# Optimization experiments

Measured on AMD Instinct MI355X. Metric: run time of the kernel, lower is better.

The kernel has to match this reference:

```python
import jax, jax.numpy as jnp
import numpy as np

B, C, H, W = 8, 128, 256, 256
WS = 8          # window_size (square)
HEADS = 4


def setup_inputs() -> dict:
    key = jax.random.key(0)
    k1, k2, k3, k4 = jax.random.split(key, 4)
    x = jax.random.normal(k1, (B, C, H, W), dtype=jnp.float32)
    # 1x1 convs are per-pixel matmuls; store weights as [out, in]
    w_qkv = jax.random.normal(k2, (3 * C, C), dtype=jnp.float32) * 0.05   # qkv conv, bias=False
    w_proj = jax.random.normal(k3, (C, C), dtype=jnp.float32) * 0.05      # proj conv weight
    b_proj = jax.random.normal(k4, (C,), dtype=jnp.float32) * 0.01        # proj conv bias
    return {"x": x, "w_qkv": w_qkv, "w_proj": w_proj, "b_proj": b_proj}


def reference(x, w_qkv, w_proj, b_proj):
    b, c, h, w = x.shape
    ws, heads = WS, HEADS
    d = c // heads
    scale = d ** -0.5
    hn, wn = h // ws, w // ws
    n = ws * ws  # tokens per window

    # unfold with kernel=stride=ws -> row-major window partition
    # [B,C,H,W] -> [B*hn*wn, C, n]
    xw = x.reshape(b, c, hn, ws, wn, ws)
    xw = xw.transpose(0, 2, 4, 1, 3, 5).reshape(b * hn * wn, c, n)

    # 1x1 conv QKV projection (no bias)
    qkv = jnp.einsum('oc,bcn->bon', w_qkv, xw)  # [Bw, 3C, n]
    q, k, v = jnp.split(qkv, 3, axis=1)
    q = q.reshape(-1, heads, d, n)
    k = k.reshape(-1, heads, d, n)
    v = v.reshape(-1, heads, d, n)

    # attn = (q^T k) * scale, softmax over keys
    attn = jax.nn.softmax(jnp.einsum('bhdn,bhdm->bhnm', q, k) * scale, axis=-1)
    out = jnp.einsum('bhnm,bhdm->bhdn', attn, v).reshape(-1, c, n)  # [Bw, C, n]

    # 1x1 proj conv with bias
    out = jnp.einsum('oc,bcn->bon', w_proj, out) + b_proj[None, :, None]

    # fold windows back: [Bw, C, n] -> [B, C, H, W]
    out = out.reshape(b, hn, wn, c, ws, ws)
    out = out.transpose(0, 3, 1, 4, 2, 5).reshape(b, c, h, w)
    return out
```

## Files before the change

kernel.cpp:

```cpp
#include <hip/hip_runtime.h>


#define HH    256
#define WWID  256
#define SCALE 0.17677669529663687f
#define LOG2E 1.44269504088896340736f

typedef float  f32x4  __attribute__((ext_vector_type(4)));
typedef __bf16 bf16x8 __attribute__((ext_vector_type(8)));
typedef __bf16 bf16x4 __attribute__((ext_vector_type(4)));
typedef __bf16 bf16x2 __attribute__((ext_vector_type(2)));
typedef short  s16x4  __attribute__((ext_vector_type(4)));

#define OT_BASE 16384

__device__ __forceinline__ s16x4 pack4(f32x4 v) {
  bf16x4 b = {(__bf16)v[0], (__bf16)v[1], (__bf16)v[2], (__bf16)v[3]};
  return __builtin_bit_cast(s16x4, b);
}

#if __has_builtin(__builtin_amdgcn_mfma_f32_16x16x16bf16_1k)
__device__ __forceinline__ f32x4 mfma16(s16x4 a, s16x4 b, f32x4 c) {
  return __builtin_amdgcn_mfma_f32_16x16x16bf16_1k(a, b, c, 0, 0, 0);
}
#else
__device__ __forceinline__ f32x4 mfma16(s16x4 a, s16x4 b, f32x4 c) {
  asm("v_mfma_f32_16x16x16_bf16 %0, %1, %2, %0" : "+v"(c) : "v"(a), "v"(b));
  return c;
}
#endif

__global__ void prep_weights(const float* __restrict__ wqkv,
                             const float* __restrict__ wproj,
                             __bf16* __restrict__ wbf) {
  int i = blockIdx.x * 256 + threadIdx.x;
  float v = (i < 49152) ? wqkv[i] : wproj[i - 49152];
  if (i < 16384) v *= SCALE * LOG2E;
  wbf[i] = (__bf16)v;
}

__global__ __launch_bounds__(256, 2)
void winattn_main(const float* __restrict__ x,
                  const __bf16* __restrict__ wqkv,
                  const __bf16* __restrict__ wproj,
                  const float* __restrict__ bproj,
                  float* __restrict__ out) {
  __shared__ __align__(16) char smem[32768];

  const int tid  = threadIdx.x;
  const int lane = tid & 63;
  const int wv   = tid >> 6;
  const int l15  = lane & 15;
  const int l4   = lane >> 4;

  const int bid = blockIdx.x;
  const int win = ((bid & 7) << 10) | (bid >> 3);
  const int b   = win >> 10;
  const int wy  = (win >> 5) & 31;
  const int wx  = win & 31;
  const int gy0 = wy * 8, gx0 = wx * 8;

  #pragma unroll
  for (int it = 0; it < 4; ++it) {
    int idx   = tid + it * 256;
    int cpair = idx >> 4;
    int r     = idx & 15;
    int ty    = r >> 1, tx4 = r & 1;
    const float* px = x + (((size_t)(b * 128 + 2 * cpair) * HH + gy0 + ty) * WWID + gx0 + tx4 * 4);
    float4 v0 = *(const float4*)px;
    float4 v1 = *(const float4*)(px + (size_t)HH * WWID);
    float a0[4] = {v0.x, v0.y, v0.z, v0.w};
    float a1[4] = {v1.x, v1.y, v1.z, v1.w};
    #pragma unroll
    for (int i = 0; i < 4; ++i) {
      int tok = ty * 8 + tx4 * 4 + i;
      bf16x2 w2 = {(__bf16)a0[i], (__bf16)a1[i]};
      int byte = (tok * 256 + cpair * 4) ^ ((tok & 15) << 4);
      *(bf16x2*)(smem + byte) = w2;
    }
  }
  __syncthreads();

  #define XT_AFRAG(mt, kt) \
    (*(const bf16x8*)(smem + ((((mt) * 16 + l15) * 256 + ((kt) * 32 + l4 * 8) * 2) ^ \
                              ((((mt) * 16 + l15) & 15) << 4))))
  #define OT_AFRAG(mt, kt) \
    (*(const bf16x8*)(smem + OT_BASE + ((((mt) * 16 + l15) * 256 + ((kt) * 32 + l4 * 8) * 2) ^ \
                              ((((mt) * 16 + l15) & 15) << 4))))

  s16x4 qb[2][4], kb[2][4];
  {
    f32x4 accQ[2][4] = {}, accK[2][4] = {};
    #pragma unroll
    for (int kt = 0; kt < 4; ++kt) {
      bf16x8 xf[4];
      #pragma unroll
      for (int mt = 0; mt < 4; ++mt) xf[mt] = XT_AFRAG(mt, kt);
      #pragma unroll
      for (int nt2 = 0; nt2 < 2; ++nt2) {
        bf16x8 wq = *(const bf16x8*)(wqkv + (size_t)(wv * 32 + nt2 * 16 + l15) * 128 + kt * 32 + l4 * 8);
        bf16x8 wk = *(const bf16x8*)(wqkv + (size_t)(128 + wv * 32 + nt2 * 16 + l15) * 128 + kt * 32 + l4 * 8);
        #pragma unroll
        for (int mt = 0; mt < 4; ++mt) {
          accQ[nt2][mt] = __builtin_amdgcn_mfma_f32_16x16x32_bf16(wq, xf[mt], accQ[nt2][mt], 0, 0, 0);
          accK[nt2][mt] = __builtin_amdgcn_mfma_f32_16x16x32_bf16(wk, xf[mt], accK[nt2][mt], 0, 0, 0);
        }
      }
    }
    #pragma unroll
    for (int nt2 = 0; nt2 < 2; ++nt2)
      #pragma unroll
      for (int mt = 0; mt < 4; ++mt) {
        qb[nt2][mt] = pack4(accQ[nt2][mt]);
        kb[nt2][mt] = pack4(accK[nt2][mt]);
      }
  }

  s16x4 vb[2][4];
  {
    f32x4 accV[2][4] = {};
    #pragma unroll
    for (int kt = 0; kt < 4; ++kt) {
      bf16x8 xf[4];
      #pragma unroll
      for (int mt = 0; mt < 4; ++mt) xf[mt] = XT_AFRAG(mt, kt);
      #pragma unroll
      for (int nt2 = 0; nt2 < 2; ++nt2) {
        bf16x8 wf = *(const bf16x8*)(wqkv + (size_t)(256 + wv * 32 + nt2 * 16 + l15) * 128 + kt * 32 + l4 * 8);
        #pragma unroll
        for (int mt = 0; mt < 4; ++mt)
          accV[nt2][mt] = __builtin_amdgcn_mfma_f32_16x16x32_bf16(xf[mt], wf, accV[nt2][mt], 0, 0, 0);
      }
    }
    #pragma unroll
    for (int nt2 = 0; nt2 < 2; ++nt2)
      #pragma unroll
      for (int mt = 0; mt < 4; ++mt) vb[nt2][mt] = pack4(accV[nt2][mt]);
  }

  f32x4 oacc[4][2] = {};
  #pragma unroll
  for (int t = 0; t < 4; ++t) {
    f32x4 st[4];
    #pragma unroll
    for (int m = 0; m < 4; ++m) {
      f32x4 z = {0.f, 0.f, 0.f, 0.f};
      st[m] = mfma16(kb[0][m], qb[0][t], z);
      st[m] = mfma16(kb[1][m], qb[1][t], st[m]);
    }
    float mx = st[0][0];
    #pragma unroll
    for (int m = 0; m < 4; ++m)
      #pragma unroll
      for (int r = 0; r < 4; ++r) mx = fmaxf(mx, st[m][r]);
    mx = fmaxf(mx, __shfl_xor(mx, 16));
    mx = fmaxf(mx, __shfl_xor(mx, 32));
    float p[4][4];
    float sm = 0.f;
    #pragma unroll
    for (int m = 0; m < 4; ++m)
      #pragma unroll
      for (int r = 0; r < 4; ++r) {
        p[m][r] = __builtin_amdgcn_exp2f(st[m][r] - mx);
        sm += p[m][r];
      }
    sm += __shfl_xor(sm, 16);
    sm += __shfl_xor(sm, 32);
    float inv = __builtin_amdgcn_rcpf(sm);
    s16x4 ap[4];
    #pragma unroll
    for (int m = 0; m < 4; ++m) {
      f32x4 pn = {p[m][0] * inv, p[m][1] * inv, p[m][2] * inv, p[m][3] * inv};
      ap[m] = pack4(pn);
    }
    #pragma unroll
    for (int m = 0; m < 4; ++m)
      #pragma unroll
      for (int n = 0; n < 2; ++n)
        oacc[t][n] = mfma16(ap[m], vb[n][m], oacc[t][n]);
  }

  #pragma unroll
  for (int t = 0; t < 4; ++t)
    #pragma unroll
    for (int n = 0; n < 2; ++n)
      #pragma unroll
      for (int r = 0; r < 4; ++r) {
        int tok  = t * 16 + l4 * 4 + r;
        int c    = wv * 32 + n * 16 + l15;
        int byte = OT_BASE + ((tok * 256 + c * 2) ^ ((tok & 15) << 4));
        *(__bf16*)(smem + byte) = (__bf16)oacc[t][n][r];
      }
  __syncthreads();

  f32x4 pacc[2][4] = {};
  #pragma unroll
  for (int kt = 0; kt < 4; ++kt) {
    bf16x8 of[4];
    #pragma unroll
    for (int mt = 0; mt < 4; ++mt) of[mt] = OT_AFRAG(mt, kt);
    #pragma unroll
    for (int i = 0; i < 2; ++i) {
      bf16x8 wp = *(const bf16x8*)(wproj + (size_t)((wv * 2 + i) * 16 + l15) * 128 + kt * 32 + l4 * 8);
      #pragma unroll
      for (int mt = 0; mt < 4; ++mt)
        pacc[i][mt] = __builtin_amdgcn_mfma_f32_16x16x32_bf16(of[mt], wp, pacc[i][mt], 0, 0, 0);
    }
  }

  #pragma unroll
  for (int i = 0; i < 2; ++i) {
    int o = (wv * 2 + i) * 16 + l15;
    float bias = bproj[o];
    float* obase = out + (size_t)(b * 128 + o) * ((size_t)HH * WWID) + gy0 * WWID + gx0;
    #pragma unroll
    for (int mt = 0; mt < 4; ++mt) {
      int tok0 = mt * 16 + l4 * 4;
      int ty = tok0 >> 3, tx0 = tok0 & 7;
      float4 f = {pacc[i][mt][0] + bias, pacc[i][mt][1] + bias,
                  pacc[i][mt][2] + bias, pacc[i][mt][3] + bias};
      *(float4*)(obase + ty * WWID + tx0) = f;
    }
  }
}

extern "C" void kernel_launch(void* const* d_in, const int* in_sizes, int n_in,
                              void* d_out, int out_size, void* d_ws, size_t ws_size,
                              hipStream_t stream) {
  const float* x     = (const float*)d_in[0];
  const float* wqkv  = (const float*)d_in[1];
  const float* wproj = (const float*)d_in[2];
  const float* bproj = (const float*)d_in[3];
  float* out = (float*)d_out;

  __bf16* wbf = (__bf16*)d_ws;
  prep_weights<<<256, 256, 0, stream>>>(wqkv, wproj, wbf);
  winattn_main<<<8192, 256, 0, stream>>>(x, wbf, wbf + 49152, bproj, out);
}
```

Measured before the change: 261.0 us.

## Process four windows per block with double-buffered prefetch of next window

Each block now handles four consecutive windows instead of one, cutting the grid from 8192 to 2048 blocks. The next window's input is loaded into registers while the projection GEMM of the current window runs, then written into an alternate LDS buffer. The attention output is stored to LDS per row tile instead of being kept in accumulators, which lowers register pressure. The cost is more LDS per block (48KB), which may reduce occupancy, plus extra barriers and a longer serial chain inside each block.

```diff
diff --git a/kernel.cpp b/kernel.cpp
--- a/kernel.cpp
+++ b/kernel.cpp
@@ -12,7 +12,7 @@
 typedef __bf16 bf16x2 __attribute__((ext_vector_type(2)));
 typedef short  s16x4  __attribute__((ext_vector_type(4)));
 
-#define OT_BASE 16384
+#define OT_BASE 32768
 
 __device__ __forceinline__ s16x4 pack4(f32x4 v) {
   bf16x4 b = {(__bf16)v[0], (__bf16)v[1], (__bf16)v[2], (__bf16)v[3]};
@@ -45,7 +45,7 @@
                   const __bf16* __restrict__ wproj,
                   const float* __restrict__ bproj,
                   float* __restrict__ out) {
-  __shared__ __align__(16) char smem[32768];
+  __shared__ __align__(16) char smem[49152];
 
   const int tid  = threadIdx.x;
   const int lane = tid & 63;
@@ -54,172 +54,205 @@
   const int l4   = lane >> 4;
 
   const int bid = blockIdx.x;
-  const int win = ((bid & 7) << 10) | (bid >> 3);
-  const int b   = win >> 10;
-  const int wy  = (win >> 5) & 31;
-  const int wx  = win & 31;
-  const int gy0 = wy * 8, gx0 = wx * 8;
-
+  const int b   = bid & 7;
+  const int grp = bid >> 3;
+
+  int tcpair[4], tty[4], ttx4[4];
   #pragma unroll
   for (int it = 0; it < 4; ++it) {
-    int idx   = tid + it * 256;
-    int cpair = idx >> 4;
-    int r     = idx & 15;
-    int ty    = r >> 1, tx4 = r & 1;
-    const float* px = x + (((size_t)(b * 128 + 2 * cpair) * HH + gy0 + ty) * WWID + gx0 + tx4 * 4);
-    float4 v0 = *(const float4*)px;
-    float4 v1 = *(const float4*)(px + (size_t)HH * WWID);
-    float a0[4] = {v0.x, v0.y, v0.z, v0.w};
-    float a1[4] = {v1.x, v1.y, v1.z, v1.w};
-    #pragma unroll
-    for (int i = 0; i < 4; ++i) {
-      int tok = ty * 8 + tx4 * 4 + i;
-      bf16x2 w2 = {(__bf16)a0[i], (__bf16)a1[i]};
-      int byte = (tok * 256 + cpair * 4) ^ ((tok & 15) << 4);
-      *(bf16x2*)(smem + byte) = w2;
-    }
+    int idx = tid + it * 256;
+    tcpair[it] = idx >> 4;
+    int r = idx & 15;
+    tty[it] = r >> 1;
+    ttx4[it] = r & 1;
   }
-  __syncthreads();
-
-  #define XT_AFRAG(mt, kt) \
-    (*(const bf16x8*)(smem + ((((mt) * 16 + l15) * 256 + ((kt) * 32 + l4 * 8) * 2) ^ \
+
+  #define ISSUE_LOADS(widx, pv0, pv1)                                              \
+    {                                                                              \
+      int gy0_ = ((widx) >> 5) * 8, gx0_ = ((widx) & 31) * 8;                      \
+      _Pragma("unroll")                                                            \
+      for (int it = 0; it < 4; ++it) {                                             \
+        const float* px = x + (((size_t)(b * 128 + 2 * tcpair[it]) * HH + gy0_ +   \
+                                tty[it]) * WWID + gx0_ + ttx4[it] * 4);            \
+        pv0[it] = *(const float4*)px;                                              \
+        pv1[it] = *(const float4*)(px + (size_t)HH * WWID);                        \
+      }                                                                            \
+    }
+
+  #define STORE_TILE(pv0, pv1, base)                                               \
+    {                                                                              \
+      _Pragma("unroll")                                                            \
+      for (int it = 0; it < 4; ++it) {                                             \
+        float a0_[4] = {pv0[it].x, pv0[it].y, pv0[it].z, pv0[it].w};               \
+        float a1_[4] = {pv1[it].x, pv1[it].y, pv1[it].z, pv1[it].w};               \
+        _Pragma("unroll")                                                          \
+        for (int i = 0; i < 4; ++i) {                                              \
+          int tok = tty[it] * 8 + ttx4[it] * 4 + i;                                \
+          bf16x2 w2 = {(__bf16)a0_[i], (__bf16)a1_[i]};                            \
+          int byte = (base) + ((tok * 256 + tcpair[it] * 4) ^ ((tok & 15) << 4));  \
+          *(bf16x2*)(smem + byte) = w2;                                            \
+        }                                                                          \
+      }                                                                            \
+    }
+
+  #define XT_AFRAG(base, mt, kt) \
+    (*(const bf16x8*)(smem + (base) + ((((mt) * 16 + l15) * 256 + ((kt) * 32 + l4 * 8) * 2) ^ \
                               ((((mt) * 16 + l15) & 15) << 4))))
   #define OT_AFRAG(mt, kt) \
     (*(const bf16x8*)(smem + OT_BASE + ((((mt) * 16 + l15) * 256 + ((kt) * 32 + l4 * 8) * 2) ^ \
                               ((((mt) * 16 + l15) & 15) << 4))))
 
-  s16x4 qb[2][4], kb[2][4];
   {
-    f32x4 accQ[2][4] = {}, accK[2][4] = {};
+    float4 pv0[4], pv1[4];
+    ISSUE_LOADS(grp * 4, pv0, pv1);
+    STORE_TILE(pv0, pv1, 0);
+  }
+  __syncthreads();
+
+  #pragma unroll
+  for (int w = 0; w < 4; ++w) {
+    const int XB = (w & 1) ? 16384 : 0;
+    const int NB = XB ^ 16384;
+    const int widx = grp * 4 + w;
+    const int gy0 = (widx >> 5) * 8, gx0 = (widx & 31) * 8;
+
+    s16x4 qb[2][4], kb[2][4];
+    {
+      f32x4 accQ[2][4] = {}, accK[2][4] = {};
+      #pragma unroll
+      for (int kt = 0; kt < 4; ++kt) {
+        bf16x8 xf[4];
+        #pragma unroll
+        for (int mt = 0; mt < 4; ++mt) xf[mt] = XT_AFRAG(XB, mt, kt);
+        #pragma unroll
+        for (int nt2 = 0; nt2 < 2; ++nt2) {
+          bf16x8 wq = *(const bf16x8*)(wqkv + (size_t)(wv * 32 + nt2 * 16 + l15) * 128 + kt * 32 + l4 * 8);
+          bf16x8 wk = *(const bf16x8*)(wqkv + (size_t)(128 + wv * 32 + nt2 * 16 + l15) * 128 + kt * 32 + l4 * 8);
+          #pragma unroll
+          for (int mt = 0; mt < 4; ++mt) {
+            accQ[nt2][mt] = __builtin_amdgcn_mfma_f32_16x16x32_bf16(wq, xf[mt], accQ[nt2][mt], 0, 0, 0);
+            accK[nt2][mt] = __builtin_amdgcn_mfma_f32_16x16x32_bf16(wk, xf[mt], accK[nt2][mt], 0, 0, 0);
+          }
+        }
+      }
+      #pragma unroll
+      for (int nt2 = 0; nt2 < 2; ++nt2)
+        #pragma unroll
+        for (int mt = 0; mt < 4; ++mt) {
+          qb[nt2][mt] = pack4(accQ[nt2][mt]);
+          kb[nt2][mt] = pack4(accK[nt2][mt]);
+        }
+    }
+
+    s16x4 vb[2][4];
+    {
+      f32x4 accV[2][4] = {};
+      #pragma unroll
+      for (int kt = 0; kt < 4; ++kt) {
+        bf16x8 xf[4];
+        #pragma unroll
+        for (int mt = 0; mt < 4; ++mt) xf[mt] = XT_AFRAG(XB, mt, kt);
+        #pragma unroll
+        for (int nt2 = 0; nt2 < 2; ++nt2) {
+          bf16x8 wf = *(const bf16x8*)(wqkv + (size_t)(256 + wv * 32 + nt2 * 16 + l15) * 128 + kt * 32 + l4 * 8);
+          #pragma unroll
+          for (int mt = 0; mt < 4; ++mt)
+            accV[nt2][mt] = __builtin_amdgcn_mfma_f32_16x16x32_bf16(xf[mt], wf, accV[nt2][mt], 0, 0, 0);
+        }
+      }
+      #pragma unroll
+      for (int nt2 = 0; nt2 < 2; ++nt2)
+        #pragma unroll
+        for (int mt = 0; mt < 4; ++mt) vb[nt2][mt] = pack4(accV[nt2][mt]);
+    }
+
+    #pragma unroll
+    for (int t = 0; t < 4; ++t) {
+      f32x4 st[4];
+      #pragma unroll
+      for (int m = 0; m < 4; ++m) {
+        f32x4 z = {0.f, 0.f, 0.f, 0.f};
+        st[m] = mfma16(kb[0][m], qb[0][t], z);
+        st[m] = mfma16(kb[1][m], qb[1][t], st[m]);
+      }
+      float mx = st[0][0];
+      #pragma unroll
+      for (int m = 0; m < 4; ++m)
+        #pragma unroll
+        for (int r = 0; r < 4; ++r) mx = fmaxf(mx, st[m][r]);
+      mx = fmaxf(mx, __shfl_xor(mx, 16));
+      mx = fmaxf(mx, __shfl_xor(mx, 32));
+      float p[4][4];
+      float sm = 0.f;
+      #pragma unroll
+      for (int m = 0; m < 4; ++m)
+        #pragma unroll
+        for (int r = 0; r < 4; ++r) {
+          p[m][r] = __builtin_amdgcn_exp2f(st[m][r] - mx);
+          sm += p[m][r];
+        }
+      sm += __shfl_xor(sm, 16);
+      sm += __shfl_xor(sm, 32);
+      float inv = __builtin_amdgcn_rcpf(sm);
+      s16x4 ap[4];
+      #pragma unroll
+      for (int m = 0; m < 4; ++m) {
+        f32x4 pn = {p[m][0] * inv, p[m][1] * inv, p[m][2] * inv, p[m][3] * inv};
+        ap[m] = pack4(pn);
+      }
+      f32x4 o0 = {0.f, 0.f, 0.f, 0.f}, o1 = {0.f, 0.f, 0.f, 0.f};
+      #pragma unroll
+      for (int m = 0; m < 4; ++m) {
+        o0 = mfma16(ap[m], vb[0][m], o0);
+        o1 = mfma16(ap[m], vb[1][m], o1);
+      }
+      #pragma unroll
+      for (int r = 0; r < 4; ++r) {
+        int tok = t * 16 + l4 * 4 + r;
+        int c0  = wv * 32 + l15;
+        int sw  = (tok & 15) << 4;
+        *(__bf16*)(smem + OT_BASE + ((tok * 256 + c0 * 2) ^ sw))        = (__bf16)o0[r];
+        *(__bf16*)(smem + OT_BASE + ((tok * 256 + (c0 + 16) * 2) ^ sw)) = (__bf16)o1[r];
+      }
+    }
+    __syncthreads();
+
+    float4 pv0[4], pv1[4];
+    if (w < 3) ISSUE_LOADS(widx + 1, pv0, pv1);
+
+    f32x4 pacc[2][4] = {};
     #pragma unroll
     for (int kt = 0; kt < 4; ++kt) {
-      bf16x8 xf[4];
-      #pragma unroll
-      for (int mt = 0; mt < 4; ++mt) xf[mt] = XT_AFRAG(mt, kt);
-      #pragma unroll
-      for (int nt2 = 0; nt2 < 2; ++nt2) {
-        bf16x8 wq = *(const bf16x8*)(wqkv + (size_t)(wv * 32 + nt2 * 16 + l15) * 128 + kt * 32 + l4 * 8);
-        bf16x8 wk = *(const bf16x8*)(wqkv + (size_t)(128 + wv * 32 + nt2 * 16 + l15) * 128 + kt * 32 + l4 * 8);
-        #pragma unroll
-        for (int mt = 0; mt < 4; ++mt) {
-          accQ[nt2][mt] = __builtin_amdgcn_mfma_f32_16x16x32_bf16(wq, xf[mt], accQ[nt2][mt], 0, 0, 0);
-          accK[nt2][mt] = __builtin_amdgcn_mfma_f32_16x16x32_bf16(wk, xf[mt], accK[nt2][mt], 0, 0, 0);
-        }
-      }
-    }
-    #pragma unroll
-    for (int nt2 = 0; nt2 < 2; ++nt2)
-      #pragma unroll
-      for (int mt = 0; mt < 4; ++mt) {
-        qb[nt2][mt] = pack4(accQ[nt2][mt]);
-        kb[nt2][mt] = pack4(accK[nt2][mt]);
-      }
-  }
-
-  s16x4 vb[2][4];
-  {
-    f32x4 accV[2][4] = {};
-    #pragma unroll
-    for (int kt = 0; kt < 4; ++kt) {
-      bf16x8 xf[4];
-      #pragma unroll
-      for (int mt = 0; mt < 4; ++mt) xf[mt] = XT_AFRAG(mt, kt);
-      #pragma unroll
-      for (int nt2 = 0; nt2 < 2; ++nt2) {
-        bf16x8 wf = *(const bf16x8*)(wqkv + (size_t)(256 + wv * 32 + nt2 * 16 + l15) * 128 + kt * 32 + l4 * 8);
+      bf16x8 of[4];
+      #pragma unroll
+      for (int mt = 0; mt < 4; ++mt) of[mt] = OT_AFRAG(mt, kt);
+      #pragma unroll
+      for (int i = 0; i < 2; ++i) {
+        bf16x8 wp = *(const bf16x8*)(wproj + (size_t)((wv * 2 + i) * 16 + l15) * 128 + kt * 32 + l4 * 8);
         #pragma unroll
         for (int mt = 0; mt < 4; ++mt)
-          accV[nt2][mt] = __builtin_amdgcn_mfma_f32_16x16x32_bf16(xf[mt], wf, accV[nt2][mt], 0, 0, 0);
-      }
-    }
-    #pragma unroll
-    for (int nt2 = 0; nt2 < 2; ++nt2)
-      #pragma unroll
-      for (int mt = 0; mt < 4; ++mt) vb[nt2][mt] = pack4(accV[nt2][mt]);
-  }
-
-  f32x4 oacc[4][2] = {};
-  #pragma unroll
-  for (int t = 0; t < 4; ++t) {
-    f32x4 st[4];
-    #pragma unroll
-    for (int m = 0; m < 4; ++m) {
-      f32x4 z = {0.f, 0.f, 0.f, 0.f};
-      st[m] = mfma16(kb[0][m], qb[0][t], z);
-      st[m] = mfma16(kb[1][m], qb[1][t], st[m]);
-    }
-    float mx = st[0][0];
-    #pragma unroll
-    for (int m = 0; m < 4; ++m)
-      #pragma unroll
-      for (int r = 0; r < 4; ++r) mx = fmaxf(mx, st[m][r]);
-    mx = fmaxf(mx, __shfl_xor(mx, 16));
-    mx = fmaxf(mx, __shfl_xor(mx, 32));
-    float p[4][4];
-    float sm = 0.f;
-    #pragma unroll
-    for (int m = 0; m < 4; ++m)
-      #pragma unroll
-      for (int r = 0; r < 4; ++r) {
-        p[m][r] = __builtin_amdgcn_exp2f(st[m][r] - mx);
-        sm += p[m][r];
-      }
-    sm += __shfl_xor(sm, 16);
-    sm += __shfl_xor(sm, 32);
-    float inv = __builtin_amdgcn_rcpf(sm);
-    s16x4 ap[4];
-    #pragma unroll
-    for (int m = 0; m < 4; ++m) {
-      f32x4 pn = {p[m][0] * inv, p[m][1] * inv, p[m][2] * inv, p[m][3] * inv};
-      ap[m] = pack4(pn);
-    }
-    #pragma unroll
-    for (int m = 0; m < 4; ++m)
-      #pragma unroll
-      for (int n = 0; n < 2; ++n)
-        oacc[t][n] = mfma16(ap[m], vb[n][m], oacc[t][n]);
-  }
-
-  #pragma unroll
-  for (int t = 0; t < 4; ++t)
-    #pragma unroll
-    for (int n = 0; n < 2; ++n)
-      #pragma unroll
-      for (int r = 0; r < 4; ++r) {
-        int tok  = t * 16 + l4 * 4 + r;
-        int c    = wv * 32 + n * 16 + l15;
-        int byte = OT_BASE + ((tok * 256 + c * 2) ^ ((tok & 15) << 4));
-        *(__bf16*)(smem + byte) = (__bf16)oacc[t][n][r];
-      }
-  __syncthreads();
-
-  f32x4 pacc[2][4] = {};
-  #pragma unroll
-  for (int kt = 0; kt < 4; ++kt) {
-    bf16x8 of[4];
-    #pragma unroll
-    for (int mt = 0; mt < 4; ++mt) of[mt] = OT_AFRAG(mt, kt);
+          pacc[i][mt] = __builtin_amdgcn_mfma_f32_16x16x32_bf16(of[mt], wp, pacc[i][mt], 0, 0, 0);
+      }
+    }
+
     #pragma unroll
     for (int i = 0; i < 2; ++i) {
-      bf16x8 wp = *(const bf16x8*)(wproj + (size_t)((wv * 2 + i) * 16 + l15) * 128 + kt * 32 + l4 * 8);
-      #pragma unroll
-      for (int mt = 0; mt < 4; ++mt)
-        pacc[i][mt] = __builtin_amdgcn_mfma_f32_16x16x32_bf16(of[mt], wp, pacc[i][mt], 0, 0, 0);
-    }
-  }
-
-  #pragma unroll
-  for (int i = 0; i < 2; ++i) {
-    int o = (wv * 2 + i) * 16 + l15;
-    float bias = bproj[o];
-    float* obase = out + (size_t)(b * 128 + o) * ((size_t)HH * WWID) + gy0 * WWID + gx0;
-    #pragma unroll
-    for (int mt = 0; mt < 4; ++mt) {
-      int tok0 = mt * 16 + l4 * 4;
-      int ty = tok0 >> 3, tx0 = tok0 & 7;
-      float4 f = {pacc[i][mt][0] + bias, pacc[i][mt][1] + bias,
-                  pacc[i][mt][2] + bias, pacc[i][mt][3] + bias};
-      *(float4*)(obase + ty * WWID + tx0) = f;
+      int o = (wv * 2 + i) * 16 + l15;
+      float bias = bproj[o];
+      float* obase = out + (size_t)(b * 128 + o) * ((size_t)HH * WWID) + gy0 * WWID + gx0;
+      #pragma unroll
+      for (int mt = 0; mt < 4; ++mt) {
+        int tok0 = mt * 16 + l4 * 4;
+        int ty = tok0 >> 3, tx0 = tok0 & 7;
+        float4 f = {pacc[i][mt][0] + bias, pacc[i][mt][1] + bias,
+                    pacc[i][mt][2] + bias, pacc[i][mt][3] + bias};
+        *(float4*)(obase + ty * WWID + tx0) = f;
+      }
+    }
+
+    if (w < 3) {
+      STORE_TILE(pv0, pv1, NB);
+      __syncthreads();
     }
   }
 }
@@ -235,5 +268,5 @@
 
   __bf16* wbf = (__bf16*)d_ws;
   prep_weights<<<256, 256, 0, stream>>>(wqkv, wproj, wbf);
-  winattn_main<<<8192, 256, 0, stream>>>(x, wbf, wbf + 49152, bproj, out);
-}
+  winattn_main<<<2048, 256, 0, stream>>>(x, wbf, wbf + 49152, bproj, out);
+}
```

After: 388.3 us. 1.49x slower.

## Defer V projection after softmax, swap PV operands for vector LDS stores, add setprio

Applied to the files above, without the earlier changes.

The V projection now runs after the softmax probabilities are computed, so Q/K and V accumulators are never live at the same time, which lowers register pressure. The PV MFMA swaps its operands so each lane holds four consecutive channels of one token, letting it write the attention output to LDS as 8-byte vector stores instead of scalar bf16 stores. MFMA clusters are wrapped in s_setprio raises to favour matrix issue across waves. The cost is that all probabilities (ap[4][4]) stay live across the V GEMM, and setprio may help or hurt the interleaving between waves.

```diff
diff --git a/kernel.cpp b/kernel.cpp
--- a/kernel.cpp
+++ b/kernel.cpp
@@ -100,11 +100,13 @@
       for (int nt2 = 0; nt2 < 2; ++nt2) {
         bf16x8 wq = *(const bf16x8*)(wqkv + (size_t)(wv * 32 + nt2 * 16 + l15) * 128 + kt * 32 + l4 * 8);
         bf16x8 wk = *(const bf16x8*)(wqkv + (size_t)(128 + wv * 32 + nt2 * 16 + l15) * 128 + kt * 32 + l4 * 8);
+        __builtin_amdgcn_s_setprio(1);
         #pragma unroll
         for (int mt = 0; mt < 4; ++mt) {
           accQ[nt2][mt] = __builtin_amdgcn_mfma_f32_16x16x32_bf16(wq, xf[mt], accQ[nt2][mt], 0, 0, 0);
           accK[nt2][mt] = __builtin_amdgcn_mfma_f32_16x16x32_bf16(wk, xf[mt], accK[nt2][mt], 0, 0, 0);
         }
+        __builtin_amdgcn_s_setprio(0);
       }
     }
     #pragma unroll
@@ -116,38 +118,18 @@
       }
   }
 
-  s16x4 vb[2][4];
-  {
-    f32x4 accV[2][4] = {};
-    #pragma unroll
-    for (int kt = 0; kt < 4; ++kt) {
-      bf16x8 xf[4];
-      #pragma unroll
-      for (int mt = 0; mt < 4; ++mt) xf[mt] = XT_AFRAG(mt, kt);
-      #pragma unroll
-      for (int nt2 = 0; nt2 < 2; ++nt2) {
-        bf16x8 wf = *(const bf16x8*)(wqkv + (size_t)(256 + wv * 32 + nt2 * 16 + l15) * 128 + kt * 32 + l4 * 8);
-        #pragma unroll
-        for (int mt = 0; mt < 4; ++mt)
-          accV[nt2][mt] = __builtin_amdgcn_mfma_f32_16x16x32_bf16(xf[mt], wf, accV[nt2][mt], 0, 0, 0);
-      }
-    }
-    #pragma unroll
-    for (int nt2 = 0; nt2 < 2; ++nt2)
-      #pragma unroll
-      for (int mt = 0; mt < 4; ++mt) vb[nt2][mt] = pack4(accV[nt2][mt]);
-  }
-
-  f32x4 oacc[4][2] = {};
+  s16x4 ap[4][4];
   #pragma unroll
   for (int t = 0; t < 4; ++t) {
     f32x4 st[4];
+    __builtin_amdgcn_s_setprio(1);
     #pragma unroll
     for (int m = 0; m < 4; ++m) {
       f32x4 z = {0.f, 0.f, 0.f, 0.f};
       st[m] = mfma16(kb[0][m], qb[0][t], z);
       st[m] = mfma16(kb[1][m], qb[1][t], st[m]);
     }
+    __builtin_amdgcn_s_setprio(0);
     float mx = st[0][0];
     #pragma unroll
     for (int m = 0; m < 4; ++m)
@@ -167,30 +149,54 @@
     sm += __shfl_xor(sm, 16);
     sm += __shfl_xor(sm, 32);
     float inv = __builtin_amdgcn_rcpf(sm);
-    s16x4 ap[4];
     #pragma unroll
     for (int m = 0; m < 4; ++m) {
       f32x4 pn = {p[m][0] * inv, p[m][1] * inv, p[m][2] * inv, p[m][3] * inv};
-      ap[m] = pack4(pn);
-    }
-    #pragma unroll
-    for (int m = 0; m < 4; ++m)
-      #pragma unroll
-      for (int n = 0; n < 2; ++n)
-        oacc[t][n] = mfma16(ap[m], vb[n][m], oacc[t][n]);
-  }
-
-  #pragma unroll
-  for (int t = 0; t < 4; ++t)
-    #pragma unroll
-    for (int n = 0; n < 2; ++n)
-      #pragma unroll
-      for (int r = 0; r < 4; ++r) {
-        int tok  = t * 16 + l4 * 4 + r;
-        int c    = wv * 32 + n * 16 + l15;
-        int byte = OT_BASE + ((tok * 256 + c * 2) ^ ((tok & 15) << 4));
-        *(__bf16*)(smem + byte) = (__bf16)oacc[t][n][r];
-      }
+      ap[t][m] = pack4(pn);
+    }
+  }
+
+  s16x4 vb[2][4];
+  {
+    f32x4 acc[2][4] = {};
+    #pragma unroll
+    for (int kt = 0; kt < 4; ++kt) {
+      bf16x8 xf[4];
+      #pragma unroll
+      for (int mt = 0; mt < 4; ++mt) xf[mt] = XT_AFRAG(mt, kt);
+      #pragma unroll
+      for (int nt2 = 0; nt2 < 2; ++nt2) {
+        bf16x8 w = *(const bf16x8*)(wqkv + (size_t)(256 + wv * 32 + nt2 * 16 + l15) * 128 + kt * 32 + l4 * 8);
+        __builtin_amdgcn_s_setprio(1);
+        #pragma unroll
+        for (int mt = 0; mt < 4; ++mt)
+          acc[nt2][mt] = __builtin_amdgcn_mfma_f32_16x16x32_bf16(xf[mt], w, acc[nt2][mt], 0, 0, 0);
+        __builtin_amdgcn_s_setprio(0);
+      }
+    }
+    #pragma unroll
+    for (int nt2 = 0; nt2 < 2; ++nt2)
+      #pragma unroll
+      for (int mt = 0; mt < 4; ++mt) vb[nt2][mt] = pack4(acc[nt2][mt]);
+  }
+
+  #pragma unroll
+  for (int t = 0; t < 4; ++t) {
+    f32x4 o0 = {0.f, 0.f, 0.f, 0.f}, o1 = {0.f, 0.f, 0.f, 0.f};
+    __builtin_amdgcn_s_setprio(1);
+    #pragma unroll
+    for (int m = 0; m < 4; ++m) {
+      o0 = mfma16(vb[0][m], ap[t][m], o0);
+      o1 = mfma16(vb[1][m], ap[t][m], o1);
+    }
+    __builtin_amdgcn_s_setprio(0);
+    int tok = t * 16 + l15;
+    int sw  = (tok & 15) << 4;
+    s16x4 p0 = pack4(o0), p1 = pack4(o1);
+    int c0 = wv * 32 + l4 * 4;
+    *(s16x4*)(smem + OT_BASE + ((tok * 256 + c0 * 2) ^ sw))          = p0;
+    *(s16x4*)(smem + OT_BASE + ((tok * 256 + (c0 + 16) * 2) ^ sw))   = p1;
+  }
   __syncthreads();
 
   f32x4 pacc[2][4] = {};
@@ -202,9 +208,11 @@
     #pragma unroll
     for (int i = 0; i < 2; ++i) {
       bf16x8 wp = *(const bf16x8*)(wproj + (size_t)((wv * 2 + i) * 16 + l15) * 128 + kt * 32 + l4 * 8);
+      __builtin_amdgcn_s_setprio(1);
       #pragma unroll
       for (int mt = 0; mt < 4; ++mt)
         pacc[i][mt] = __builtin_amdgcn_mfma_f32_16x16x32_bf16(of[mt], wp, pacc[i][mt], 0, 0, 0);
+      __builtin_amdgcn_s_setprio(0);
     }
   }
 
```

Measured after the change: 249.4 us. 1.05x faster.
